# Kernel tuning notes

Hardware: AMD Instinct MI355X
Metric: run time of the kernel (lower is better)

## Reference

```python
import jax, jax.numpy as jnp
import numpy as np

B = 2
C = 96
NH = 4
HD = C // NH
DEPTH = 2
LAT, LON = 181, 360
WH, WW = 6, 12
N = WH * WW
PT, PBm, PL, PR = 2, 3, 0, 0
H, W = LAT + PT + PBm, LON + PL + PR
SH, SW = WH // 2, WW // 2
NWH, NWW = H // WH, W // WW
NW = NWH * NWW
SCALE = HD ** -0.5

def _rel_index():
    ch, cw = np.meshgrid(np.arange(WH), np.arange(WW), indexing='ij')
    coords = np.stack([ch, cw]).reshape(2, -1)
    rel = (coords[:, :, None] - coords[:, None, :]).transpose(1, 2, 0).astype(np.int64)
    rel[:, :, 0] += WH - 1
    rel[:, :, 1] += WW - 1
    rel[:, :, 0] *= 2 * WW - 1
    return rel.sum(-1)  # (N, N)

REL_IDX = jnp.asarray(_rel_index())

def _shift_mask():
    img = np.zeros((H, W))
    cnt = 0
    for hs in (slice(0, -WH), slice(-WH, -SH), slice(-SH, None)):
        for ws in (slice(0, -WW), slice(-WW, -SW), slice(-SW, None)):
            img[hs, ws] = cnt
            cnt += 1
    mw = img.reshape(NWH, WH, NWW, WW).transpose(0, 2, 1, 3).reshape(NW, N)
    am = mw[:, None, :] - mw[:, :, None]
    return np.where(am != 0, -100.0, 0.0).astype(np.float32)

ATTN_MASK = jnp.asarray(_shift_mask())  # (NW, N, N)

def _ln(x, g, b):
    m = x.mean(-1, keepdims=True)
    v = x.var(-1, keepdims=True)
    return (x - m) * jax.lax.rsqrt(v + 1e-5) * g + b

def _win_part(x):
    b = x.shape[0]
    return x.reshape(b, NWH, WH, NWW, WW, C).transpose(0, 1, 3, 2, 4, 5).reshape(-1, N, C)

def _win_rev(xw, b):
    return xw.reshape(b, NWH, NWW, WH, WW, C).transpose(0, 1, 3, 2, 4, 5).reshape(b, H, W, C)

def _block(x, shift, g1, b1, qw, qb, pw, pb, rpb, g2, b2, f1w, f1b, f2w, f2b):
    b = x.shape[0]
    sc = x
    x = _ln(x, g1, b1)
    if shift:
        x = jnp.roll(x, (-SH, -SW), (1, 2))
    xw = _win_part(x)  # (b*NW, N, C)
    qkv = (xw @ qw.T + qb).reshape(-1, N, 3, NH, HD).transpose(2, 0, 3, 1, 4)
    q, k, v = qkv[0], qkv[1], qkv[2]  # each (b*NW, NH, N, HD)
    attn = (q * SCALE) @ k.transpose(0, 1, 3, 2)  # (b*NW, NH, N, N)
    bias = rpb[REL_IDX].transpose(2, 0, 1)  # (NH, N, N)
    attn = attn + bias[None]
    if shift:
        attn = (attn.reshape(b, NW, NH, N, N) + ATTN_MASK[None, :, None]).reshape(-1, NH, N, N)
    attn = jax.nn.softmax(attn, axis=-1)
    out = (attn @ v).transpose(0, 2, 1, 3).reshape(-1, N, C)
    out = out @ pw.T + pb
    x = _win_rev(out, b)
    if shift:
        x = jnp.roll(x, (SH, SW), (1, 2))
    x = sc + x
    h = _ln(x, g2, b2)
    h = jax.nn.gelu(h @ f1w.T + f1b) @ f2w.T + f2b
    return x + h

def _forward(x, g1, b1, qkv_w, qkv_b, proj_w, proj_b, rpb, g2, b2, fc1_w, fc1_b, fc2_w, fc2_b):
    x = jnp.pad(x, ((0, 0), (0, 0), (PT, PBm), (PL, PR)))  # ZeroPad2d
    x = x.transpose(0, 2, 3, 1)  # (B, H, W, C)
    for i in range(DEPTH):
        x = _block(x, i % 2 == 1, g1[i], b1[i], qkv_w[i], qkv_b[i], proj_w[i], proj_b[i],
                   rpb[i], g2[i], b2[i], fc1_w[i], fc1_b[i], fc2_w[i], fc2_b[i])
    x = x.transpose(0, 3, 1, 2)
    return x[:, :, PT:H - PBm, PL:W - PR]


def setup_inputs() -> dict:
    key = jax.random.key(0)
    ks = jax.random.split(key, 6)
    s = 0.02
    tbl = (2 * WH - 1) * (2 * WW - 1)
    return {
        'x': jax.random.normal(ks[0], (B, C, LAT, LON), jnp.float32),
        'g1': jnp.ones((DEPTH, C), jnp.float32),
        'b1': jnp.zeros((DEPTH, C), jnp.float32),
        'qkv_w': jax.random.normal(ks[1], (DEPTH, 3 * C, C), jnp.float32) * s,
        'qkv_b': jnp.zeros((DEPTH, 3 * C), jnp.float32),
        'proj_w': jax.random.normal(ks[2], (DEPTH, C, C), jnp.float32) * s,
        'proj_b': jnp.zeros((DEPTH, C), jnp.float32),
        'rpb': jax.random.normal(ks[3], (DEPTH, tbl, NH), jnp.float32) * s,
        'g2': jnp.ones((DEPTH, C), jnp.float32),
        'b2': jnp.zeros((DEPTH, C), jnp.float32),
        'fc1_w': jax.random.normal(ks[4], (DEPTH, 4 * C, C), jnp.float32) * s,
        'fc1_b': jnp.zeros((DEPTH, 4 * C), jnp.float32),
        'fc2_w': jax.random.normal(ks[5], (DEPTH, C, 4 * C), jnp.float32) * s,
        'fc2_b': jnp.zeros((DEPTH, C), jnp.float32),
    }


def reference(x, g1, b1, qkv_w, qkv_b, proj_w, proj_b, rpb, g2, b2, fc1_w, fc1_b, fc2_w, fc2_b):
    return _forward(x, g1, b1, qkv_w, qkv_b, proj_w, proj_b, rpb, g2, b2, fc1_w, fc1_b, fc2_w, fc2_b)
```

## Files before the change

kernel.cpp:

```cpp
#include <hip/hip_runtime.h>
#include <hip/hip_bf16.h>
#include <math.h>

#define BB    2
#define CC    96
#define NHD   4
#define HDIM  24
#define LAT_  181
#define LON_  360
#define PT_   2
#define HH    186
#define WWID  360
#define WH_   6
#define WW_   12
#define NTOK  72
#define SH_   3
#define SW_   6
#define NWH_  31
#define NWW_  30
#define NWIN  930
#define SCALE_ 0.20412414523193154f

typedef __attribute__((ext_vector_type(8))) short short8v;
typedef __attribute__((ext_vector_type(4))) float f32x4;

__device__ __forceinline__ unsigned short pk_bf16(float x) {
    __hip_bfloat16 h = __float2bfloat16(x);
    union { __hip_bfloat16 b; unsigned short u; } cv; cv.b = h; return cv.u;
}
__device__ __forceinline__ uint2 pk4(float a, float b, float c, float d) {
    __hip_bfloat162 lo = __float22bfloat162_rn(make_float2(a, b));
    __hip_bfloat162 hi = __float22bfloat162_rn(make_float2(c, d));
    union { __hip_bfloat162 b; unsigned u; } c0, c1; c0.b = lo; c1.b = hi;
    uint2 r; r.x = c0.u; r.y = c1.u; return r;
}

__global__ __launch_bounds__(256) void k_pad2(const float* __restrict__ in, float* __restrict__ X) {
    int bid = blockIdx.x;
    int ct = bid % 3; bid /= 3;
    int wt = bid % 12; bid /= 12;
    int h = bid % HH; int b = bid / HH;
    int lat = h - PT_;
    int tx = threadIdx.x & 31, ty = threadIdx.x >> 5;
    __shared__ float tile[32][33];
    if (lat >= 0 && lat < LAT_) {
        int w = wt * 32 + tx;
        #pragma unroll
        for (int i = 0; i < 4; ++i) {
            int c = ct * 32 + ty + 8 * i;
            float v = 0.f;
            if (w < WWID) v = in[((long)(b * CC + c)) * (LAT_ * LON_) + lat * LON_ + w];
            tile[ty + 8 * i][tx] = v;
        }
    } else {
        #pragma unroll
        for (int i = 0; i < 4; ++i) tile[ty + 8 * i][tx] = 0.f;
    }
    __syncthreads();
    #pragma unroll
    for (int i = 0; i < 4; ++i) {
        int w = wt * 32 + ty + 8 * i;
        if (w < WWID)
            X[(((long)(b * HH + h)) * WWID + w) * CC + ct * 32 + tx] = tile[tx][ty + 8 * i];
    }
}

__global__ __launch_bounds__(256) void k_crop2(const float* __restrict__ X, float* __restrict__ out) {
    int bid = blockIdx.x;
    int ct = bid % 3; bid /= 3;
    int wt = bid % 12; bid /= 12;
    int lat = bid % LAT_; int b = bid / LAT_;
    int h = lat + PT_;
    int tx = threadIdx.x & 31, ty = threadIdx.x >> 5;
    __shared__ float tile[32][33];
    #pragma unroll
    for (int i = 0; i < 4; ++i) {
        int w = wt * 32 + ty + 8 * i;
        if (w < WWID)
            tile[ty + 8 * i][tx] = X[(((long)(b * HH + h)) * WWID + w) * CC + ct * 32 + tx];
    }
    __syncthreads();
    {
        int w = wt * 32 + tx;
        if (w < WWID) {
            #pragma unroll
            for (int i = 0; i < 4; ++i) {
                int c = ct * 32 + ty + 8 * i;
                out[((long)(b * CC + c)) * (LAT_ * LON_) + lat * LON_ + w] = tile[tx][ty + 8 * i];
            }
        }
    }
}

__global__ void k_wprep(const float* __restrict__ f1w, const float* __restrict__ f2w,
                        const float* __restrict__ qkvw, const float* __restrict__ projw,
                        const float* __restrict__ rpb,
                        unsigned short* __restrict__ wbf, float* __restrict__ biasg) {
    int id = blockIdx.x * 256 + threadIdx.x;
    if (id < 73728) {
        int layer = id / 36864, rem = id % 36864;
        int ks = rem / 12288, r2 = rem % 12288;
        int nt = r2 / 512, r3 = r2 % 512;
        int lane = r3 / 8, e = r3 % 8;
        int o = nt * 16 + (lane & 15);
        int c = ks * 32 + 8 * (lane >> 4) + e;
        wbf[(long)layer * 36864 + rem] = pk_bf16(f1w[((long)layer * 384 + o) * 96 + c]);
    } else if (id < 147456) {
        int id2 = id - 73728;
        int layer = id2 / 36864, rem = id2 % 36864;
        int ks = rem / 3072, r2 = rem % 3072;
        int nt = r2 / 512, r3 = r2 % 512;
        int lane = r3 / 8, e = r3 % 8;
        int o = nt * 16 + (lane & 15);
        int c = ks * 32 + 8 * (lane >> 4) + e;
        wbf[73728 + (long)layer * 36864 + rem] = pk_bf16(f2w[((long)layer * 96 + o) * 384 + c]);
    } else if (id < 202752) {
        wbf[id] = pk_bf16(qkvw[id - 147456]);
    } else if (id < 221184) {
        wbf[id] = pk_bf16(projw[id - 202752]);
    } else {
        int id2 = id - 221184;
        int layer = id2 / 102400, r = id2 % 102400;
        int type = r / 25600; r %= 25600;
        int h = r / 6400; r %= 6400;
        int i = r / 80, j = r % 80;
        float v;
        if (i >= 72 || j >= 72) {
            v = -10000.f;
        } else {
            int thi = i / 12, twi = i % 12, thj = j / 12, twj = j % 12;
            int ridx = (thi - thj + 5) * 23 + (twi - twj + 11);
            v = rpb[(layer * 253 + ridx) * 4 + h];
            if (layer == 1) {
                int eh = type & 1, ew = type >> 1;
                int ri = (eh ? (thi < 3 ? 1 : 2) * 3 : 0) + (ew ? (twi < 6 ? 1 : 2) : 0);
                int rj = (eh ? (thj < 3 ? 1 : 2) * 3 : 0) + (ew ? (twj < 6 ? 1 : 2) : 0);
                if (ri != rj) v -= 100.f;
            }
        }
        biasg[id2] = v;
    }
}

template <int SHIFT>
__global__ __launch_bounds__(1024, 8) void k_attn(float* __restrict__ X,
        const float* __restrict__ gg, const float* __restrict__ bb,
        const unsigned short* __restrict__ wqkv, const float* __restrict__ qkvb,
        const unsigned short* __restrict__ wprj, const float* __restrict__ projb,
        const float* __restrict__ biasT) {
    __shared__ __align__(16) unsigned char smem[73984];
    unsigned short* As  = (unsigned short*)smem;
    unsigned short* os  = (unsigned short*)smem;
    unsigned short* qs  = (unsigned short*)(smem + 16640);
    unsigned short* ks  = (unsigned short*)(smem + 32000);
    unsigned short* vt  = (unsigned short*)(smem + 47360);

    int bid = blockIdx.x;
    int b = bid / NWIN, wi = bid % NWIN;
    int nwh = wi / NWW_, nww = wi % NWW_;
    int tid = threadIdx.x;
    int wv = tid >> 6, lane = tid & 63;
    int li = lane & 15, gq = lane >> 4;

    int type = SHIFT ? ((nwh == 30 ? 1 : 0) | (nww == 29 ? 2 : 0)) : 0;
    const float* bias_t = biasT + type * 25600;

    {
        unsigned* vz = (unsigned*)vt;
        for (int idx = tid; idx < 6656; idx += 1024) vz[idx] = 0u;
        unsigned* az = (unsigned*)(As + 72 * 104);
        for (int idx = tid; idx < 416; idx += 1024) az[idx] = 0u;
    }

    {
        int sub = lane >> 3, p = lane & 7;
        int t = wv * 8 + sub;
        if (t < 72) {
            int th = t / 12, tw = t % 12;
            int hr = nwh * WH_ + th, wr = nww * WW_ + tw;
            int ho = SHIFT ? (hr + SH_) % HH : hr;
            int wo = SHIFT ? (wr + SW_) % WWID : wr;
            const float* xr = X + (((long)b * HH + ho) * WWID + wo) * CC;
            float4 a  = *(const float4*)(xr + p * 4);
            float4 c4 = *(const float4*)(xr + p * 4 + 32);
            float4 e4 = *(const float4*)(xr + p * 4 + 64);
            float s  = a.x + a.y + a.z + a.w + c4.x + c4.y + c4.z + c4.w + e4.x + e4.y + e4.z + e4.w;
            float sq = a.x*a.x + a.y*a.y + a.z*a.z + a.w*a.w + c4.x*c4.x + c4.y*c4.y + c4.z*c4.z + c4.w*c4.w
                     + e4.x*e4.x + e4.y*e4.y + e4.z*e4.z + e4.w*e4.w;
            #pragma unroll
            for (int off = 1; off < 8; off <<= 1) {
                s  += __shfl_xor(s, off);
                sq += __shfl_xor(sq, off);
            }
            float mean = s * (1.f / CC);
            float var = sq * (1.f / CC) - mean * mean;
            float rs = rsqrtf(var + 1e-5f);
            float4 g0 = *(const float4*)(gg + p * 4);
            float4 g1v = *(const float4*)(gg + p * 4 + 32);
            float4 g2v = *(const float4*)(gg + p * 4 + 64);
            float4 t0 = *(const float4*)(bb + p * 4);
            float4 t1 = *(const float4*)(bb + p * 4 + 32);
            float4 t2 = *(const float4*)(bb + p * 4 + 64);
            *(uint2*)(As + t * 104 + p * 4) =
                pk4((a.x - mean) * rs * g0.x + t0.x, (a.y - mean) * rs * g0.y + t0.y,
                    (a.z - mean) * rs * g0.z + t0.z, (a.w - mean) * rs * g0.w + t0.w);
            *(uint2*)(As + t * 104 + p * 4 + 32) =
                pk4((c4.x - mean) * rs * g1v.x + t1.x, (c4.y - mean) * rs * g1v.y + t1.y,
                    (c4.z - mean) * rs * g1v.z + t1.z, (c4.w - mean) * rs * g1v.w + t1.w);
            *(uint2*)(As + t * 104 + p * 4 + 64) =
                pk4((e4.x - mean) * rs * g2v.x + t2.x, (e4.y - mean) * rs * g2v.y + t2.y,
                    (e4.z - mean) * rs * g2v.z + t2.z, (e4.w - mean) * rs * g2v.w + t2.w);
        }
    }
    __syncthreads();

    for (int mt = wv; mt < 18; mt += 16) {
        short8v aw[3];
        #pragma unroll
        for (int ksi = 0; ksi < 3; ++ksi)
            aw[ksi] = *(const short8v*)(wqkv + (mt * 16 + li) * 96 + ksi * 32 + 8 * gq);
        float bias4[4];
        #pragma unroll
        for (int r = 0; r < 4; ++r) bias4[r] = qkvb[mt * 16 + 4 * gq + r];
        f32x4 acc[5];
        #pragma unroll
        for (int nt = 0; nt < 5; ++nt) acc[nt] = (f32x4){0.f, 0.f, 0.f, 0.f};
        #pragma unroll
        for (int nt = 0; nt < 5; ++nt)
            #pragma unroll
            for (int ksi = 0; ksi < 3; ++ksi) {
                short8v by = *(const short8v*)(As + (nt * 16 + li) * 104 + ksi * 32 + 8 * gq);
                acc[nt] = __builtin_amdgcn_mfma_f32_16x16x32_bf16(aw[ksi], by, acc[nt], 0, 0, 0);
            }
        int which = mt / 6, mtl = mt % 6;
        int oo0 = mtl * 16 + 4 * gq;
        int h = oo0 / 24, d0 = oo0 % 24;
        #pragma unroll
        for (int nt = 0; nt < 5; ++nt) {
            int token = nt * 16 + li;
            if (which == 2) {
                #pragma unroll
                for (int r = 0; r < 4; ++r)
                    vt[(h * 32 + d0 + r) * 104 + token] = pk_bf16(acc[nt][r] + bias4[r]);
            } else {
                float v0 = acc[nt][0] + bias4[0], v1 = acc[nt][1] + bias4[1];
                float v2 = acc[nt][2] + bias4[2], v3 = acc[nt][3] + bias4[3];
                if (which == 0) { v0 *= SCALE_; v1 *= SCALE_; v2 *= SCALE_; v3 *= SCALE_; }
                unsigned short* dst = (which == 0 ? qs : ks) + (h * 80 + token) * 24 + d0;
                *(uint2*)dst = pk4(v0, v1, v2, v3);
            }
        }
    }
    __syncthreads();

    for (int u = wv; u < 20; u += 16) {
        int h = u / 5, nt = u % 5;
        short8v bq = {0,0,0,0,0,0,0,0};
        if (gq < 3) bq = *(const short8v*)(qs + (h * 80 + nt * 16 + li) * 24 + 8 * gq);
        const float* brow = bias_t + (h * 80 + nt * 16 + li) * 80;
        float p[20];
        float sum = 0.f;
        #pragma unroll
        for (int mt = 0; mt < 5; ++mt) {
            short8v ak = {0,0,0,0,0,0,0,0};
            if (gq < 3) ak = *(const short8v*)(ks + (h * 80 + mt * 16 + li) * 24 + 8 * gq);
            f32x4 ct = __builtin_amdgcn_mfma_f32_16x16x32_bf16(ak, bq, (f32x4){0.f,0.f,0.f,0.f}, 0, 0, 0);
            float4 bv = *(const float4*)(brow + mt * 16 + 4 * gq);
            p[mt*4+0] = __expf(ct[0] + bv.x);
            p[mt*4+1] = __expf(ct[1] + bv.y);
            p[mt*4+2] = __expf(ct[2] + bv.z);
            p[mt*4+3] = __expf(ct[3] + bv.w);
            sum += p[mt*4+0] + p[mt*4+1] + p[mt*4+2] + p[mt*4+3];
        }
        sum += __shfl_xor(sum, 16);
        sum += __shfl_xor(sum, 32);
        float inv = sum > 0.f ? 1.f / sum : 0.f;
        #pragma unroll
        for (int k2 = 0; k2 < 20; ++k2) p[k2] *= inv;

        short8v ap[3];
        #pragma unroll
        for (int ksi = 0; ksi < 3; ++ksi) {
            float pv[8];
            #pragma unroll
            for (int e = 0; e < 8; ++e) {
                int srcl = li + 16 * (2 * (gq & 1) + (e >> 2));
                float s0 = __shfl(p[8 * ksi + (e & 3)], srcl);
                float s1 = (ksi < 2) ? __shfl(p[8 * ksi + 4 + (e & 3)], srcl) : 0.f;
                pv[e] = (gq >= 2) ? s1 : s0;
            }
            uint2 lo = pk4(pv[0], pv[1], pv[2], pv[3]);
            uint2 hi = pk4(pv[4], pv[5], pv[6], pv[7]);
            union { uint4 u; short8v s; } cvt;
            cvt.u = make_uint4(lo.x, lo.y, hi.x, hi.y);
            ap[ksi] = cvt.s;
        }
        #pragma unroll
        for (int nt2 = 0; nt2 < 2; ++nt2) {
            f32x4 acc = (f32x4){0.f, 0.f, 0.f, 0.f};
            #pragma unroll
            for (int ksi = 0; ksi < 3; ++ksi) {
                short8v bv2 = *(const short8v*)(vt + (h * 32 + nt2 * 16 + li) * 104 + ksi * 32 + 8 * gq);
                acc = __builtin_amdgcn_mfma_f32_16x16x32_bf16(ap[ksi], bv2, acc, 0, 0, 0);
            }
            int d = nt2 * 16 + li;
            if (d < 24) {
                #pragma unroll
                for (int r = 0; r < 4; ++r)
                    os[(nt * 16 + 4 * gq + r) * 104 + h * 24 + d] = pk_bf16(acc[r]);
            }
        }
    }
    __syncthreads();

    for (int u = wv; u < 30; u += 16) {
        int mt = u / 6, nt = u % 6;
        f32x4 acc = (f32x4){0.f, 0.f, 0.f, 0.f};
        #pragma unroll
        for (int ksi = 0; ksi < 3; ++ksi) {
            short8v ao = *(const short8v*)(os + (mt * 16 + li) * 104 + ksi * 32 + 8 * gq);
            short8v bw = *(const short8v*)(wprj + (nt * 16 + li) * 96 + ksi * 32 + 8 * gq);
            acc = __builtin_amdgcn_mfma_f32_16x16x32_bf16(ao, bw, acc, 0, 0, 0);
        }
        int o = nt * 16 + li;
        float bo = projb[o];
        #pragma unroll
        for (int r = 0; r < 4; ++r) {
            int token = mt * 16 + 4 * gq + r;
            if (token < 72) {
                int th = token / 12, tw = token % 12;
                int hr = nwh * WH_ + th, wr = nww * WW_ + tw;
                int ho = SHIFT ? (hr + SH_) % HH : hr;
                int wo = SHIFT ? (wr + SW_) % WWID : wr;
                X[(((long)b * HH + ho) * WWID + wo) * CC + o] += acc[r] + bo;
            }
        }
    }
}

__global__ __launch_bounds__(256, 4) void k_mlp_mfma(float* __restrict__ X,
        const float* __restrict__ g, const float* __restrict__ bta,
        const unsigned short* __restrict__ w1f, const float* __restrict__ b1v,
        const unsigned short* __restrict__ w2f, const float* __restrict__ b2v) {
    __shared__ __align__(16) unsigned short As[32 * 120];
    __shared__ __align__(16) unsigned short Hs[32 * 392];
    long tok0 = (long)blockIdx.x * 32;
    int tid = threadIdx.x;

    {
        int t = tid >> 3, p = tid & 7;
        const float* xr = X + (tok0 + t) * CC;
        float4 a = *(const float4*)(xr + p * 4);
        float4 b = *(const float4*)(xr + p * 4 + 32);
        float4 c4 = *(const float4*)(xr + p * 4 + 64);
        float s  = a.x + a.y + a.z + a.w + b.x + b.y + b.z + b.w + c4.x + c4.y + c4.z + c4.w;
        float sq = a.x*a.x + a.y*a.y + a.z*a.z + a.w*a.w + b.x*b.x + b.y*b.y + b.z*b.z + b.w*b.w
                 + c4.x*c4.x + c4.y*c4.y + c4.z*c4.z + c4.w*c4.w;
        #pragma unroll
        for (int off = 1; off < 8; off <<= 1) {
            s  += __shfl_xor(s, off);
            sq += __shfl_xor(sq, off);
        }
        float mean = s * (1.f / CC);
        float var = sq * (1.f / CC) - mean * mean;
        float rs = rsqrtf(var + 1e-5f);
        float4 g0 = *(const float4*)(g + p * 4);
        float4 g1 = *(const float4*)(g + p * 4 + 32);
        float4 g2 = *(const float4*)(g + p * 4 + 64);
        float4 t0 = *(const float4*)(bta + p * 4);
        float4 t1 = *(const float4*)(bta + p * 4 + 32);
        float4 t2 = *(const float4*)(bta + p * 4 + 64);
        unsigned short* arow = As + t * 120;
        *(uint2*)(arow + p * 4) =
            pk4((a.x - mean) * rs * g0.x + t0.x, (a.y - mean) * rs * g0.y + t0.y,
                (a.z - mean) * rs * g0.z + t0.z, (a.w - mean) * rs * g0.w + t0.w);
        *(uint2*)(arow + p * 4 + 32) =
            pk4((b.x - mean) * rs * g1.x + t1.x, (b.y - mean) * rs * g1.y + t1.y,
                (b.z - mean) * rs * g1.z + t1.z, (b.w - mean) * rs * g1.w + t1.w);
        *(uint2*)(arow + p * 4 + 64) =
            pk4((c4.x - mean) * rs * g2.x + t2.x, (c4.y - mean) * rs * g2.y + t2.y,
                (c4.z - mean) * rs * g2.z + t2.z, (c4.w - mean) * rs * g2.w + t2.w);
    }
    __syncthreads();

    int w = tid >> 6, lane = tid & 63;
    int wm = w & 1;
    int row = wm * 16 + (lane & 15);
    int kbase = 8 * (lane >> 4);

    {
        int wnh = w >> 1;
        short8v afr[3];
        #pragma unroll
        for (int ks = 0; ks < 3; ++ks)
            afr[ks] = *(const short8v*)(As + row * 120 + ks * 32 + kbase);
        f32x4 acc[12];
        #pragma unroll
        for (int j = 0; j < 12; ++j) acc[j] = (f32x4){0.f, 0.f, 0.f, 0.f};
        const short8v* wb = (const short8v*)w1f;
        #pragma unroll
        for (int j = 0; j < 12; ++j) {
            int nt = wnh * 12 + j;
            #pragma unroll
            for (int ks = 0; ks < 3; ++ks) {
                short8v bfr = wb[(ks * 24 + nt) * 64 + lane];
                acc[j] = __builtin_amdgcn_mfma_f32_16x16x32_bf16(afr[ks], bfr, acc[j], 0, 0, 0);
            }
        }
        #pragma unroll
        for (int j = 0; j < 12; ++j) {
            int n = (wnh * 12 + j) * 16 + (lane & 15);
            float bb = b1v[n];
            #pragma unroll
            for (int r = 0; r < 4; ++r) {
                float s = acc[j][r] + bb;
                float z = s + 0.044715f * s * s * s;
                float gl = s / (1.f + __expf(-1.5957691216057308f * z));
                Hs[(wm * 16 + 4 * (lane >> 4) + r) * 392 + n] = pk_bf16(gl);
            }
        }
    }
    __syncthreads();

    {
        int wnt0 = (w >> 1) * 3;
        f32x4 acc2[3];
        #pragma unroll
        for (int j = 0; j < 3; ++j) acc2[j] = (f32x4){0.f, 0.f, 0.f, 0.f};
        const short8v* wb2 = (const short8v*)w2f;
        #pragma unroll
        for (int ks = 0; ks < 12; ++ks) {
            short8v a2 = *(const short8v*)(Hs + row * 392 + ks * 32 + kbase);
            #pragma unroll
            for (int j = 0; j < 3; ++j) {
                short8v bfr = wb2[(ks * 6 + wnt0 + j) * 64 + lane];
                acc2[j] = __builtin_amdgcn_mfma_f32_16x16x32_bf16(a2, bfr, acc2[j], 0, 0, 0);
            }
        }
        #pragma unroll
        for (int j = 0; j < 3; ++j) {
            int n = (wnt0 + j) * 16 + (lane & 15);
            float bb = b2v[n];
            #pragma unroll
            for (int r = 0; r < 4; ++r) {
                long tok = tok0 + wm * 16 + 4 * (lane >> 4) + r;
                X[tok * CC + n] += acc2[j][r] + bb;
            }
        }
    }
}

extern "C" void kernel_launch(void* const* d_in, const int* in_sizes, int n_in,
                              void* d_out, int out_size, void* d_ws, size_t ws_size,
                              hipStream_t stream) {
    const float* x     = (const float*)d_in[0];
    const float* g1    = (const float*)d_in[1];
    const float* b1    = (const float*)d_in[2];
    const float* qkvw  = (const float*)d_in[3];
    const float* qkvb  = (const float*)d_in[4];
    const float* projw = (const float*)d_in[5];
    const float* projb = (const float*)d_in[6];
    const float* rpb   = (const float*)d_in[7];
    const float* g2    = (const float*)d_in[8];
    const float* b2    = (const float*)d_in[9];
    const float* f1w   = (const float*)d_in[10];
    const float* f1b   = (const float*)d_in[11];
    const float* f2w   = (const float*)d_in[12];
    const float* f2b   = (const float*)d_in[13];

    float* X = (float*)d_ws;
    unsigned short* wbf = (unsigned short*)(X + (long)BB * HH * WWID * CC);
    float* biasg = (float*)(wbf + 221184);

    const int ntok = BB * HH * WWID;

    k_pad2<<<BB * HH * 12 * 3, 256, 0, stream>>>(x, X);
    k_wprep<<<1664, 256, 0, stream>>>(f1w, f2w, qkvw, projw, rpb, wbf, biasg);

    for (int i = 0; i < 2; ++i) {
        const unsigned short* wqkv_bf = wbf + 147456 + (long)i * 27648;
        const unsigned short* wprj_bf = wbf + 202752 + (long)i * 9216;
        if (i == 0) {
            k_attn<0><<<BB * NWIN, 1024, 0, stream>>>(X, g1, b1,
                wqkv_bf, qkvb, wprj_bf, projb, biasg);
        } else {
            k_attn<1><<<BB * NWIN, 1024, 0, stream>>>(X, g1 + CC, b1 + CC,
                wqkv_bf, qkvb + 3 * CC, wprj_bf, projb + CC, biasg + 102400);
        }
        k_mlp_mfma<<<ntok / 32, 256, 0, stream>>>(X,
            g2 + i * CC, b2 + i * CC,
            wbf + (long)i * 36864, f1b + i * 4 * CC,
            wbf + 73728 + (long)i * 36864, f2b + i * CC);
    }

    k_crop2<<<BB * LAT_ * 12 * 3, 256, 0, stream>>>(X, (float*)d_out);
}
```

Before: 306.0 us.

## Enlarge MLP token tile to 64 and keep weight fragments in registers

New measurement: 300.5 us. About the same (-1.8%).

```diff
diff --git a/kernel.cpp b/kernel.cpp
--- a/kernel.cpp
+++ b/kernel.cpp
@@ -20,6 +20,7 @@
 #define NWW_  30
 #define NWIN  930
 #define SCALE_ 0.20412414523193154f
+#define MTOK  64
 
 typedef __attribute__((ext_vector_type(8))) short short8v;
 typedef __attribute__((ext_vector_type(4))) float f32x4;
@@ -338,18 +339,21 @@
     }
 }
 
-__global__ __launch_bounds__(256, 4) void k_mlp_mfma(float* __restrict__ X,
+__global__ __launch_bounds__(512, 4) void k_mlp2(float* __restrict__ X, int ntok,
         const float* __restrict__ g, const float* __restrict__ bta,
         const unsigned short* __restrict__ w1f, const float* __restrict__ b1v,
         const unsigned short* __restrict__ w2f, const float* __restrict__ b2v) {
-    __shared__ __align__(16) unsigned short As[32 * 120];
-    __shared__ __align__(16) unsigned short Hs[32 * 392];
-    long tok0 = (long)blockIdx.x * 32;
+    __shared__ __align__(16) unsigned short As[MTOK * 120];
+    __shared__ __align__(16) unsigned short Hs[MTOK * 392];
+    long tok0 = (long)blockIdx.x * MTOK;
     int tid = threadIdx.x;
+    int wv = tid >> 6, lane = tid & 63;
+    int li = lane & 15, gq = lane >> 4;
 
     {
         int t = tid >> 3, p = tid & 7;
-        const float* xr = X + (tok0 + t) * CC;
+        long gt = tok0 + t; if (gt >= ntok) gt = ntok - 1;
+        const float* xr = X + gt * CC;
         float4 a = *(const float4*)(xr + p * 4);
         float4 b = *(const float4*)(xr + p * 4 + 32);
         float4 c4 = *(const float4*)(xr + p * 4 + 64);
@@ -383,68 +387,62 @@
     }
     __syncthreads();
 
-    int w = tid >> 6, lane = tid & 63;
-    int wm = w & 1;
-    int row = wm * 16 + (lane & 15);
-    int kbase = 8 * (lane >> 4);
-
     {
-        int wnh = w >> 1;
-        short8v afr[3];
-        #pragma unroll
-        for (int ks = 0; ks < 3; ++ks)
-            afr[ks] = *(const short8v*)(As + row * 120 + ks * 32 + kbase);
-        f32x4 acc[12];
-        #pragma unroll
-        for (int j = 0; j < 12; ++j) acc[j] = (f32x4){0.f, 0.f, 0.f, 0.f};
         const short8v* wb = (const short8v*)w1f;
-        #pragma unroll
-        for (int j = 0; j < 12; ++j) {
-            int nt = wnh * 12 + j;
-            #pragma unroll
-            for (int ks = 0; ks < 3; ++ks) {
-                short8v bfr = wb[(ks * 24 + nt) * 64 + lane];
-                acc[j] = __builtin_amdgcn_mfma_f32_16x16x32_bf16(afr[ks], bfr, acc[j], 0, 0, 0);
-            }
-        }
-        #pragma unroll
-        for (int j = 0; j < 12; ++j) {
-            int n = (wnh * 12 + j) * 16 + (lane & 15);
-            float bb = b1v[n];
+        short8v bfr[3][3];
+        #pragma unroll
+        for (int j = 0; j < 3; ++j)
+            #pragma unroll
+            for (int ks = 0; ks < 3; ++ks)
+                bfr[j][ks] = wb[(ks * 24 + wv * 3 + j) * 64 + lane];
+        float bb[3];
+        #pragma unroll
+        for (int j = 0; j < 3; ++j) bb[j] = b1v[(wv * 3 + j) * 16 + li];
+        #pragma unroll
+        for (int s = 0; s < 4; ++s) {
+            short8v afr[3];
+            #pragma unroll
+            for (int ks = 0; ks < 3; ++ks)
+                afr[ks] = *(const short8v*)(As + (s * 16 + li) * 120 + ks * 32 + 8 * gq);
+            #pragma unroll
+            for (int j = 0; j < 3; ++j) {
+                f32x4 acc = (f32x4){0.f, 0.f, 0.f, 0.f};
+                #pragma unroll
+                for (int ks = 0; ks < 3; ++ks)
+                    acc = __builtin_amdgcn_mfma_f32_16x16x32_bf16(afr[ks], bfr[j][ks], acc, 0, 0, 0);
+                int n = (wv * 3 + j) * 16 + li;
+                #pragma unroll
+                for (int r = 0; r < 4; ++r) {
+                    float sv = acc[r] + bb[j];
+                    float z = sv + 0.044715f * sv * sv * sv;
+                    float gl = sv / (1.f + __expf(-1.5957691216057308f * z));
+                    Hs[(s * 16 + 4 * gq + r) * 392 + n] = pk_bf16(gl);
+                }
+            }
+        }
+    }
+    __syncthreads();
+
+    if (wv < 6) {
+        const short8v* wb2 = (const short8v*)w2f;
+        short8v bfr2[12];
+        #pragma unroll
+        for (int ks = 0; ks < 12; ++ks)
+            bfr2[ks] = wb2[(ks * 6 + wv) * 64 + lane];
+        int n = wv * 16 + li;
+        float bb = b2v[n];
+        #pragma unroll
+        for (int s = 0; s < 4; ++s) {
+            f32x4 acc = (f32x4){0.f, 0.f, 0.f, 0.f};
+            #pragma unroll
+            for (int ks = 0; ks < 12; ++ks) {
+                short8v a2 = *(const short8v*)(Hs + (s * 16 + li) * 392 + ks * 32 + 8 * gq);
+                acc = __builtin_amdgcn_mfma_f32_16x16x32_bf16(a2, bfr2[ks], acc, 0, 0, 0);
+            }
             #pragma unroll
             for (int r = 0; r < 4; ++r) {
-                float s = acc[j][r] + bb;
-                float z = s + 0.044715f * s * s * s;
-                float gl = s / (1.f + __expf(-1.5957691216057308f * z));
-                Hs[(wm * 16 + 4 * (lane >> 4) + r) * 392 + n] = pk_bf16(gl);
-            }
-        }
-    }
-    __syncthreads();
-
-    {
-        int wnt0 = (w >> 1) * 3;
-        f32x4 acc2[3];
-        #pragma unroll
-        for (int j = 0; j < 3; ++j) acc2[j] = (f32x4){0.f, 0.f, 0.f, 0.f};
-        const short8v* wb2 = (const short8v*)w2f;
-        #pragma unroll
-        for (int ks = 0; ks < 12; ++ks) {
-            short8v a2 = *(const short8v*)(Hs + row * 392 + ks * 32 + kbase);
-            #pragma unroll
-            for (int j = 0; j < 3; ++j) {
-                short8v bfr = wb2[(ks * 6 + wnt0 + j) * 64 + lane];
-                acc2[j] = __builtin_amdgcn_mfma_f32_16x16x32_bf16(a2, bfr, acc2[j], 0, 0, 0);
-            }
-        }
-        #pragma unroll
-        for (int j = 0; j < 3; ++j) {
-            int n = (wnt0 + j) * 16 + (lane & 15);
-            float bb = b2v[n];
-            #pragma unroll
-            for (int r = 0; r < 4; ++r) {
-                long tok = tok0 + wm * 16 + 4 * (lane >> 4) + r;
-                X[tok * CC + n] += acc2[j][r] + bb;
+                long gt = tok0 + s * 16 + 4 * gq + r;
+                if (gt < ntok) X[gt * CC + n] += acc[r] + bb;
             }
         }
     }
@@ -473,6 +471,7 @@
     float* biasg = (float*)(wbf + 221184);
 
     const int ntok = BB * HH * WWID;
+    const int mlp_blocks = (ntok + MTOK - 1) / MTOK;
 
     k_pad2<<<BB * HH * 12 * 3, 256, 0, stream>>>(x, X);
     k_wprep<<<1664, 256, 0, stream>>>(f1w, f2w, qkvw, projw, rpb, wbf, biasg);
@@ -487,7 +486,7 @@
             k_attn<1><<<BB * NWIN, 1024, 0, stream>>>(X, g1 + CC, b1 + CC,
                 wqkv_bf, qkvb + 3 * CC, wprj_bf, projb + CC, biasg + 102400);
         }
-        k_mlp_mfma<<<ntok / 32, 256, 0, stream>>>(X,
+        k_mlp2<<<mlp_blocks, 512, 0, stream>>>(X, ntok,
             g2 + i * CC, b2 + i * CC,
             wbf + (long)i * 36864, f1b + i * 4 * CC,
             wbf + 73728 + (long)i * 36864, f2b + i * CC);
```
